# Performance work log

Measured on AMD Instinct MI355X. Metric: run time of the kernel, lower is better.

Reference implementation:

```python
import jax, jax.numpy as jnp
import numpy as np

N = 32768          # number of points
K = 64             # max_num_neighbors
D = 3              # spatial dim (3x3 local frames)
R = 1.0            # radius
TARGET_DEG = 48.0  # desired mean neighborhood size


def _radius_graph_numpy(pos, r, k):
    """Padded radius neighbor search (mimics torch_cluster.radius, incl. self-loop).

    Returns (edge_src, edge_dst, num_neighbors); padded slots have src == dst so
    edge_vec = 0 and they contribute nothing to the covariance scatter.
    """
    n = pos.shape[0]
    nbr = np.full((n, k), -1, dtype=np.int64)
    r2 = r * r
    chunk = 2048
    for s in range(0, n, chunk):
        q = pos[s:s + chunk]                                   # [C, D]
        d2 = ((q[:, None, :] - pos[None, :, :]) ** 2).sum(-1)  # [C, N]
        d2m = np.where(d2 <= r2, d2, np.inf)
        idx = np.argpartition(d2m, k - 1, axis=1)[:, :k]       # k nearest candidates
        dsel = np.take_along_axis(d2m, idx, axis=1)
        nbr[s:s + chunk] = np.where(np.isfinite(dsel), idx, -1)
    num_neighbors = (nbr >= 0).sum(axis=1).astype(np.int32)
    edge_dst = np.repeat(np.arange(n, dtype=np.int64), k)
    edge_src = nbr.reshape(-1)
    edge_src = np.where(edge_src >= 0, edge_src, edge_dst)     # pad: src == dst
    return edge_src.astype(np.int32), edge_dst.astype(np.int32), num_neighbors


def setup_inputs() -> dict:
    rng = np.random.default_rng(0)
    # box size so that density * (4/3) pi r^3 ~= TARGET_DEG
    L = (N * (4.0 / 3.0) * np.pi * R ** 3 / TARGET_DEG) ** (1.0 / 3.0)
    pos = rng.uniform(0.0, L, size=(N, D)).astype(np.float32)
    edge_src, edge_dst, num_neighbors = _radius_graph_numpy(pos, R, K)
    return {
        "pos": jnp.asarray(pos),
        "edge_src": jnp.asarray(edge_src),
        "edge_dst": jnp.asarray(edge_dst),
        "num_neighbors": jnp.asarray(num_neighbors),
    }


def reference(pos, edge_src, edge_dst, num_neighbors):
    n = pos.shape[0]
    # edge_vec = pos[col] - pos[row]; padded edges (src==dst) give exact zeros
    ev = pos[edge_src] - pos[edge_dst]                         # [E, 3]
    outer = ev[:, :, None] * ev[:, None, :]                    # [E, 3, 3]
    cov = jax.ops.segment_sum(outer, edge_dst, num_segments=n)  # [N, 3, 3]

    no_nbr = num_neighbors <= 1                                # self-loop only
    # replace degenerate (zero) covariances with a distinct-eigenvalue matrix so
    # eigh is well-defined; these rows are zeroed afterwards (exceptional 'zero').
    safe = jnp.diag(jnp.arange(1.0, D + 1.0, dtype=pos.dtype))
    cov = jnp.where(no_nbr[:, None, None], safe, cov)

    _, vecs = jnp.linalg.eigh(cov)                             # [N, 3, 3] columns = eigvecs
    frames = vecs.transpose(0, 2, 1)                           # rows = eigvecs
    frames = jnp.where(no_nbr[:, None, None], 0.0, frames)
    return frames


if __name__ == "__main__":
    out = reference(**setup_inputs())
    print(out.shape, out.dtype)
```

## Files before the change

kernel.cpp:

```cpp
#include <hip/hip_runtime.h>
#include <math.h>


#pragma clang fp contract(off)

#define EPS_F32    5.9604645e-8f
#define SAFMIN_F32 1.17549435e-38f

__device__ __forceinline__ float lapy2f(float x, float y) {
#pragma clang fp contract(off)
  float xa = fabsf(x), ya = fabsf(y);
  float w = fmaxf(xa, ya);
  float z = fminf(xa, ya);
  if (z == 0.0f) return w;
  float t = z / w;
  return w * sqrtf(1.0f + t * t);
}

__device__ __forceinline__ void slartgf(float f, float g, float* c, float* s, float* r) {
#pragma clang fp contract(off)
  const float safmin = SAFMIN_F32;
  const float safmax = 8.50705917e37f;
  const float rtmin  = 1.08420217e-19f;
  const float rtmax  = 6.52530446e18f;
  if (g == 0.0f) { *c = 1.0f; *s = 0.0f; *r = f; return; }
  if (f == 0.0f) { *c = 0.0f; *s = copysignf(1.0f, g); *r = fabsf(g); return; }
  float f1 = fabsf(f), g1 = fabsf(g);
  if (f1 > rtmin && f1 < rtmax && g1 > rtmin && g1 < rtmax) {
    float d = sqrtf(f * f + g * g);
    *c = f1 / d;
    *r = copysignf(d, f);
    *s = g / (*r);
  } else {
    float u  = fminf(safmax, fmaxf(safmin, fmaxf(f1, g1)));
    float fs = f / u, gs = g / u;
    float d  = sqrtf(fs * fs + gs * gs);
    *c = fabsf(fs) / d;
    float rr = copysignf(d, f);
    *s = gs / rr;
    *r = rr * u;
  }
}

__device__ __forceinline__ void slaev2f(float a, float b, float c,
                                        float* rt1, float* rt2,
                                        float* cs1, float* sn1) {
#pragma clang fp contract(off)
  float sm  = a + c;
  float df  = a - c;
  float adf = fabsf(df);
  float tb  = b + b;
  float ab  = fabsf(tb);
  float acmx, acmn;
  if (fabsf(a) > fabsf(c)) { acmx = a; acmn = c; } else { acmx = c; acmn = a; }
  float rt;
  if (adf > ab)      { float t = ab / adf; rt = adf * sqrtf(1.0f + t * t); }
  else if (adf < ab) { float t = adf / ab; rt = ab  * sqrtf(1.0f + t * t); }
  else               { rt = ab * sqrtf(2.0f); }
  int sgn1;
  if (sm < 0.0f) {
    *rt1 = 0.5f * (sm - rt); sgn1 = -1;
    *rt2 = (acmx / *rt1) * acmn - (b / *rt1) * b;
  } else if (sm > 0.0f) {
    *rt1 = 0.5f * (sm + rt); sgn1 = 1;
    *rt2 = (acmx / *rt1) * acmn - (b / *rt1) * b;
  } else {
    *rt1 = 0.5f * rt; *rt2 = -0.5f * rt; sgn1 = 1;
  }
  int sgn2; float cs;
  if (df >= 0.0f) { cs = df + rt; sgn2 = 1; }
  else            { cs = df - rt; sgn2 = -1; }
  float acs = fabsf(cs);
  if (acs > ab) {
    float ct = -tb / cs;
    *sn1 = 1.0f / sqrtf(1.0f + ct * ct);
    *cs1 = ct * (*sn1);
  } else {
    if (ab == 0.0f) { *cs1 = 1.0f; *sn1 = 0.0f; }
    else {
      float tn = -cs / tb;
      *cs1 = 1.0f / sqrtf(1.0f + tn * tn);
      *sn1 = tn * (*cs1);
    }
  }
  if (sgn1 == sgn2) { float tn = *cs1; *cs1 = -(*sn1); *sn1 = tn; }
}

template <int STR>
__device__ void ssteqr3(float* S) {
#pragma clang fp contract(off)
#define D_(i)   S[((i)-1)*STR]
#define E_(i)   S[(3+(i)-1)*STR]
#define Z_(i,j) S[(5+((i)-1)*3+((j)-1))*STR]
#define WC_(q)  S[(14+(q))*STR]
#define WS_(q)  S[(16+(q))*STR]
  const int   n      = 3;
  const float eps    = EPS_F32;
  const float eps2   = eps * eps;
  const float safmin = SAFMIN_F32;
  const float ssfmax = sqrtf(8.50705917e37f) / 3.0f;
  const float ssfmin = sqrtf(safmin) / eps2;

  int   l1, l, m, lsv, lend, lendsv, iscale, nmaxit, jtot;
  float anorm, p, g, r, rt1, rt2, c, s, f, b;

  for (int q = 0; q < 9; ++q) S[(5 + q) * STR] = 0.0f;
  Z_(1, 1) = 1.0f; Z_(2, 2) = 1.0f; Z_(3, 3) = 1.0f;

  nmaxit = n * 30;
  jtot   = 0;
  l1     = 1;

L10:
  if (l1 > n) goto L160;
  if (l1 > 1) E_(l1 - 1) = 0.0f;
  if (l1 <= n - 1) {
    for (m = l1; m <= n - 1; m++) {
      float tst = fabsf(E_(m));
      if (tst == 0.0f) goto L30;
      if (tst <= (sqrtf(fabsf(D_(m))) * sqrtf(fabsf(D_(m + 1)))) * eps) {
        E_(m) = 0.0f;
        goto L30;
      }
    }
  }
  m = n;
L30:
  l = l1; lsv = l; lend = m; lendsv = lend; l1 = m + 1;
  if (lend == l) goto L10;

  anorm = 0.0f;
  for (int q = l; q <= lend; q++)     anorm = fmaxf(anorm, fabsf(D_(q)));
  for (int q = l; q <= lend - 1; q++) anorm = fmaxf(anorm, fabsf(E_(q)));
  iscale = 0;
  if (anorm == 0.0f) goto L10;
  if (anorm > ssfmax) {
    iscale = 1;
    float sc = ssfmax / anorm;
    for (int q = l; q <= lend; q++)     D_(q) *= sc;
    for (int q = l; q <= lend - 1; q++) E_(q) *= sc;
  } else if (anorm < ssfmin) {
    iscale = 2;
    float sc = ssfmin / anorm;
    for (int q = l; q <= lend; q++)     D_(q) *= sc;
    for (int q = l; q <= lend - 1; q++) E_(q) *= sc;
  }

  if (fabsf(D_(lend)) < fabsf(D_(l))) { lend = lsv; l = lendsv; }

  if (lend > l) {
L40:
    if (l != lend) {
      for (m = l; m <= lend - 1; m++) {
        float tst = E_(m) * E_(m);
        if (tst <= (eps2 * fabsf(D_(m))) * fabsf(D_(m + 1)) + safmin) goto L60;
      }
    }
    m = lend;
L60:
    if (m < lend) E_(m) = 0.0f;
    p = D_(l);
    if (m == l) goto L80;
    if (m == l + 1) {
      slaev2f(D_(l), E_(l), D_(l + 1), &rt1, &rt2, &c, &s);
      WC_(l - 1) = c;
      WS_(l - 1) = s;
      for (int row = 1; row <= n; row++) {
        float t = Z_(row, l + 1);
        Z_(row, l + 1) = c * t - s * Z_(row, l);
        Z_(row, l)     = s * t + c * Z_(row, l);
      }
      D_(l) = rt1; D_(l + 1) = rt2; E_(l) = 0.0f;
      l += 2;
      if (l <= lend) goto L40;
      goto L140;
    }
    if (jtot == nmaxit) goto L140;
    jtot++;
    g = (D_(l + 1) - p) / (2.0f * E_(l));
    r = lapy2f(g, 1.0f);
    g = D_(m) - p + (E_(l) / (g + copysignf(r, g)));
    s = 1.0f; c = 1.0f; p = 0.0f;
    for (int i = m - 1; i >= l; i--) {
      f = s * E_(i);
      b = c * E_(i);
      slartgf(g, f, &c, &s, &r);
      if (i != m - 1) E_(i + 1) = r;
      g = D_(i + 1) - p;
      r = (D_(i) - g) * s + 2.0f * c * b;
      p = s * r;
      D_(i + 1) = g + p;
      g = c * r - b;
      WC_(i - 1) = c;
      WS_(i - 1) = -s;
    }
    {
      int mm = m - l + 1;
      for (int j = mm - 1; j >= 1; j--) {
        float cj = WC_(l + j - 2);
        float sj = WS_(l + j - 2);
        if (cj != 1.0f || sj != 0.0f) {
          int col = l + j - 1;
          for (int row = 1; row <= n; row++) {
            float t = Z_(row, col + 1);
            Z_(row, col + 1) = cj * t - sj * Z_(row, col);
            Z_(row, col)     = sj * t + cj * Z_(row, col);
          }
        }
      }
    }
    D_(l) = D_(l) - p;
    E_(l) = g;
    goto L40;
L80:
    D_(l) = p;
    l++;
    if (l <= lend) goto L40;
    goto L140;
  } else {
L90:
    if (l != lend) {
      for (m = l; m >= lend + 1; m--) {
        float tst = E_(m - 1) * E_(m - 1);
        if (tst <= (eps2 * fabsf(D_(m))) * fabsf(D_(m - 1)) + safmin) goto L110;
      }
    }
    m = lend;
L110:
    if (m > lend) E_(m - 1) = 0.0f;
    p = D_(l);
    if (m == l) goto L130;
    if (m == l - 1) {
      slaev2f(D_(l - 1), E_(l - 1), D_(l), &rt1, &rt2, &c, &s);
      WC_(m - 1) = c;
      WS_(m - 1) = s;
      for (int row = 1; row <= n; row++) {
        float t = Z_(row, l);
        Z_(row, l)     = c * t - s * Z_(row, l - 1);
        Z_(row, l - 1) = s * t + c * Z_(row, l - 1);
      }
      D_(l - 1) = rt1; D_(l) = rt2; E_(l - 1) = 0.0f;
      l -= 2;
      if (l >= lend) goto L90;
      goto L140;
    }
    if (jtot == nmaxit) goto L140;
    jtot++;
    g = (D_(l - 1) - p) / (2.0f * E_(l - 1));
    r = lapy2f(g, 1.0f);
    g = D_(m) - p + (E_(l - 1) / (g + copysignf(r, g)));
    s = 1.0f; c = 1.0f; p = 0.0f;
    for (int i = m; i <= l - 1; i++) {
      f = s * E_(i);
      b = c * E_(i);
      slartgf(g, f, &c, &s, &r);
      if (i != m) E_(i - 1) = r;
      g = D_(i) - p;
      r = (D_(i + 1) - g) * s + 2.0f * c * b;
      p = s * r;
      D_(i) = g + p;
      g = c * r - b;
      WC_(i - 1) = c;
      WS_(i - 1) = s;
    }
    {
      int mm = l - m + 1;
      for (int j = 1; j <= mm - 1; j++) {
        float cj = WC_(m + j - 2);
        float sj = WS_(m + j - 2);
        if (cj != 1.0f || sj != 0.0f) {
          int col = m + j - 1;
          for (int row = 1; row <= n; row++) {
            float t = Z_(row, col + 1);
            Z_(row, col + 1) = cj * t - sj * Z_(row, col);
            Z_(row, col)     = sj * t + cj * Z_(row, col);
          }
        }
      }
    }
    D_(l) = D_(l) - p;
    E_(l - 1) = g;
    goto L90;
L130:
    D_(l) = p;
    l--;
    if (l >= lend) goto L90;
    goto L140;
  }

L140:
  if (iscale == 1) {
    float sc = anorm / ssfmax;
    for (int q = lsv; q <= lendsv; q++)     D_(q) *= sc;
    for (int q = lsv; q <= lendsv - 1; q++) E_(q) *= sc;
  } else if (iscale == 2) {
    float sc = anorm / ssfmin;
    for (int q = lsv; q <= lendsv; q++)     D_(q) *= sc;
    for (int q = lsv; q <= lendsv - 1; q++) E_(q) *= sc;
  }
  if (jtot < nmaxit) goto L10;
  goto L160;

L160:
  for (int ii = 2; ii <= n; ii++) {
    int i = ii - 1, kk = i;
    p = D_(i);
    for (int j = ii; j <= n; j++) {
      if (D_(j) < p) { kk = j; p = D_(j); }
    }
    if (kk != i) {
      D_(kk) = D_(i);
      D_(i)  = p;
      for (int row = 1; row <= n; row++) {
        float t = Z_(row, i);
        Z_(row, i)  = Z_(row, kk);
        Z_(row, kk) = t;
      }
    }
  }
#undef D_
#undef E_
#undef Z_
#undef WC_
#undef WS_
}

template <int STR>
__device__ __forceinline__ void eig_frames(float c00, float c01, float c02,
                                           float c11, float c12, float c22,
                                           float* __restrict__ o, float* S) {
#pragma clang fp contract(off)
#define SZ(idx) S[(5 + (idx)) * STR]
  float tau1, v2;
  {
    float a11 = c00, a21 = c01, a31 = c02, a22 = c11, a32 = c12, a33 = c22;
    float xnorm = fabsf(a31);
    if (xnorm == 0.0f) {
      tau1 = 0.0f; v2 = 0.0f;
      S[0 * STR] = a11; S[1 * STR] = a22; S[2 * STR] = a33;
      S[3 * STR] = a21; S[4 * STR] = a32;
    } else {
      float py2  = lapy2f(a21, xnorm);
      float beta = -copysignf(py2, a21);
      tau1 = (beta - a21) / beta;
      v2   = a31 * (1.0f / (a21 - beta));
      float t2 = a32 * v2;
      float w1 = __builtin_fmaf(tau1, t2, tau1 * a22);
      float w2 = __builtin_fmaf(tau1 * v2, a33, tau1 * a32);
      float dot = __builtin_fmaf(v2, w2, w1);
      float ac = (-0.5f * tau1) * dot;
      w1 = w1 + ac;
      w2 = __builtin_fmaf(ac, v2, w2);
      float A11 = a22 - w1;
      A11 = A11 - w1;
      float A21 = a32 - w2;
      A21 = __builtin_fmaf(-w1, v2, A21);
      float A33 = __builtin_fmaf(-v2, w2, a33);
      A33 = __builtin_fmaf(-w2, v2, A33);
      S[0 * STR] = a11;
      S[1 * STR] = A11;
      S[4 * STR] = A21;
      S[2 * STR] = A33;
      S[3 * STR] = beta;
    }
  }

  ssteqr3<STR>(S);

  if (tau1 != 0.0f) {
    #pragma unroll
    for (int j = 0; j < 3; ++j) {
      float z2 = SZ(3 + j), z3 = SZ(6 + j);
      float w  = z2 + z3 * v2;
      float t  = tau1 * w;
      SZ(3 + j) = __builtin_fmaf(-tau1, w, z2);
      SZ(6 + j) = __builtin_fmaf(v2, -t, z3);
    }
  }

  o[0] = SZ(0); o[1] = SZ(3); o[2] = SZ(6);
  o[3] = SZ(1); o[4] = SZ(4); o[5] = SZ(7);
  o[6] = SZ(2); o[7] = SZ(5); o[8] = SZ(8);
#undef SZ
}

#define NODES_PER_BLOCK 64
#define NODE_STRIDE     193
#define SOLVER_LANES    16

__global__ void __launch_bounds__(256)
pca_frames_tiled_kernel(const float* __restrict__ pos,
                        const int*   __restrict__ esrc,
                        const int*   __restrict__ nn,
                        float*       __restrict__ out,
                        int n)
{
#pragma clang fp contract(off)
  __shared__ float sev[NODES_PER_BLOCK * NODE_STRIDE];
  __shared__ float sstate[4 * 18 * SOLVER_LANES];

  const int tid   = threadIdx.x;
  const int node0 = blockIdx.x * NODES_PER_BLOCK;

  const int ebase = blockIdx.x * (NODES_PER_BLOCK * 64);
  #pragma unroll
  for (int q = 0; q < 16; ++q) {
    int eb  = q * 256 + tid;
    int n_b = eb >> 6;
    int j   = eb & 63;
    int i   = node0 + n_b;
    int s   = esrc[ebase + eb];
    float dx = pos[3 * s + 0] - pos[3 * i + 0];
    float dy = pos[3 * s + 1] - pos[3 * i + 1];
    float dz = pos[3 * s + 2] - pos[3 * i + 2];
    float* row = sev + n_b * NODE_STRIDE + 3 * j;
    row[0] = dx;
    row[1] = dy;
    row[2] = dz;
  }

  __syncthreads();

  const int w = tid >> 6;
  const int l = tid & 63;
  if (l < SOLVER_LANES) {
    int nb = w * SOLVER_LANES + l;
    int i  = node0 + nb;
    float* o = out + (size_t)i * 9;

    if (nn[i] <= 1) {
      #pragma unroll
      for (int j = 0; j < 9; ++j) o[j] = 0.0f;
      return;
    }

    const float* row = sev + nb * NODE_STRIDE;
    float c00 = 0.0f, c01 = 0.0f, c02 = 0.0f, c11 = 0.0f, c12 = 0.0f, c22 = 0.0f;
    for (int j = 0; j < 64; ++j) {
      float dx = row[3 * j + 0];
      float dy = row[3 * j + 1];
      float dz = row[3 * j + 2];
      c00 = c00 + dx * dx;
      c01 = c01 + dx * dy;
      c02 = c02 + dx * dz;
      c11 = c11 + dy * dy;
      c12 = c12 + dy * dz;
      c22 = c22 + dz * dz;
    }

    float* S = sstate + w * (18 * SOLVER_LANES) + l;
    eig_frames<SOLVER_LANES>(c00, c01, c02, c11, c12, c22, o, S);
  }
}

__global__ void __launch_bounds__(64)
pca_frames_fused_kernel(const float* __restrict__ pos,
                        const int*   __restrict__ esrc,
                        const int*   __restrict__ nn,
                        float*       __restrict__ out,
                        int n, int k)
{
#pragma clang fp contract(off)
  __shared__ float fstate[64 * 18];
  int i = blockIdx.x * blockDim.x + threadIdx.x;
  if (i >= n) return;
  float* o = out + (size_t)i * 9;

  if (nn[i] <= 1) {
    #pragma unroll
    for (int j = 0; j < 9; ++j) o[j] = 0.0f;
    return;
  }

  float px = pos[3 * i + 0], py = pos[3 * i + 1], pz = pos[3 * i + 2];
  float c00 = 0.0f, c01 = 0.0f, c02 = 0.0f, c11 = 0.0f, c12 = 0.0f, c22 = 0.0f;
  const int* ep = esrc + (size_t)i * k;
  for (int j = 0; j < k; ++j) {
    int sidx = ep[j];
    float dx = pos[3 * sidx + 0] - px;
    float dy = pos[3 * sidx + 1] - py;
    float dz = pos[3 * sidx + 2] - pz;
    c00 = c00 + dx * dx;
    c01 = c01 + dx * dy;
    c02 = c02 + dx * dz;
    c11 = c11 + dy * dy;
    c12 = c12 + dy * dz;
    c22 = c22 + dz * dz;
  }

  float* S = fstate + threadIdx.x;
  eig_frames<64>(c00, c01, c02, c11, c12, c22, o, S);
}

extern "C" void kernel_launch(void* const* d_in, const int* in_sizes, int n_in,
                              void* d_out, int out_size, void* d_ws, size_t ws_size,
                              hipStream_t stream) {
  const float* pos  = (const float*)d_in[0];
  const int*   esrc = (const int*)d_in[1];
  const int*   nn   = (const int*)d_in[3];
  float*       out  = (float*)d_out;

  int n = in_sizes[0] / 3;
  if (n <= 0) return;
  int k = in_sizes[1] / n;

  if (k == 64 && (n % NODES_PER_BLOCK) == 0) {
    hipLaunchKernelGGL(pca_frames_tiled_kernel, dim3(n / NODES_PER_BLOCK),
                       dim3(256), 0, stream, pos, esrc, nn, out, n);
  } else {
    const int block = 64;
    hipLaunchKernelGGL(pca_frames_fused_kernel, dim3((n + block - 1) / block),
                       dim3(block), 0, stream, pos, esrc, nn, out, n, k);
  }
}
```

Baseline: 104.6 us.

## Keep 3x3 tridiagonal QL eigen-solver state in registers instead of shared memory

Rewrites the ssteqr-style 3x3 eigen-solver so D, E, Z and the rotation buffers live in scalar registers, selected through ternary macros, instead of strided shared-memory slots. This removes the per-thread shared-memory state arrays and the LDS traffic inside the iterative solver. It also loads the neighbor position as one 12-byte struct. The dynamic indices become select chains, which can add ALU work and raise register pressure.

Measured after the change: 115.4 us. 10.3% more time.

```diff
diff --git a/kernel.cpp b/kernel.cpp
--- a/kernel.cpp
+++ b/kernel.cpp
@@ -86,259 +86,18 @@
   if (sgn1 == sgn2) { float tn = *cs1; *cs1 = -(*sn1); *sn1 = tn; }
 }
 
-template <int STR>
-__device__ void ssteqr3(float* S) {
-#pragma clang fp contract(off)
-#define D_(i)   S[((i)-1)*STR]
-#define E_(i)   S[(3+(i)-1)*STR]
-#define Z_(i,j) S[(5+((i)-1)*3+((j)-1))*STR]
-#define WC_(q)  S[(14+(q))*STR]
-#define WS_(q)  S[(16+(q))*STR]
-  const int   n      = 3;
-  const float eps    = EPS_F32;
-  const float eps2   = eps * eps;
-  const float safmin = SAFMIN_F32;
-  const float ssfmax = sqrtf(8.50705917e37f) / 3.0f;
-  const float ssfmin = sqrtf(safmin) / eps2;
-
-  int   l1, l, m, lsv, lend, lendsv, iscale, nmaxit, jtot;
-  float anorm, p, g, r, rt1, rt2, c, s, f, b;
-
-  for (int q = 0; q < 9; ++q) S[(5 + q) * STR] = 0.0f;
-  Z_(1, 1) = 1.0f; Z_(2, 2) = 1.0f; Z_(3, 3) = 1.0f;
-
-  nmaxit = n * 30;
-  jtot   = 0;
-  l1     = 1;
-
-L10:
-  if (l1 > n) goto L160;
-  if (l1 > 1) E_(l1 - 1) = 0.0f;
-  if (l1 <= n - 1) {
-    for (m = l1; m <= n - 1; m++) {
-      float tst = fabsf(E_(m));
-      if (tst == 0.0f) goto L30;
-      if (tst <= (sqrtf(fabsf(D_(m))) * sqrtf(fabsf(D_(m + 1)))) * eps) {
-        E_(m) = 0.0f;
-        goto L30;
-      }
-    }
-  }
-  m = n;
-L30:
-  l = l1; lsv = l; lend = m; lendsv = lend; l1 = m + 1;
-  if (lend == l) goto L10;
-
-  anorm = 0.0f;
-  for (int q = l; q <= lend; q++)     anorm = fmaxf(anorm, fabsf(D_(q)));
-  for (int q = l; q <= lend - 1; q++) anorm = fmaxf(anorm, fabsf(E_(q)));
-  iscale = 0;
-  if (anorm == 0.0f) goto L10;
-  if (anorm > ssfmax) {
-    iscale = 1;
-    float sc = ssfmax / anorm;
-    for (int q = l; q <= lend; q++)     D_(q) *= sc;
-    for (int q = l; q <= lend - 1; q++) E_(q) *= sc;
-  } else if (anorm < ssfmin) {
-    iscale = 2;
-    float sc = ssfmin / anorm;
-    for (int q = l; q <= lend; q++)     D_(q) *= sc;
-    for (int q = l; q <= lend - 1; q++) E_(q) *= sc;
-  }
-
-  if (fabsf(D_(lend)) < fabsf(D_(l))) { lend = lsv; l = lendsv; }
-
-  if (lend > l) {
-L40:
-    if (l != lend) {
-      for (m = l; m <= lend - 1; m++) {
-        float tst = E_(m) * E_(m);
-        if (tst <= (eps2 * fabsf(D_(m))) * fabsf(D_(m + 1)) + safmin) goto L60;
-      }
-    }
-    m = lend;
-L60:
-    if (m < lend) E_(m) = 0.0f;
-    p = D_(l);
-    if (m == l) goto L80;
-    if (m == l + 1) {
-      slaev2f(D_(l), E_(l), D_(l + 1), &rt1, &rt2, &c, &s);
-      WC_(l - 1) = c;
-      WS_(l - 1) = s;
-      for (int row = 1; row <= n; row++) {
-        float t = Z_(row, l + 1);
-        Z_(row, l + 1) = c * t - s * Z_(row, l);
-        Z_(row, l)     = s * t + c * Z_(row, l);
-      }
-      D_(l) = rt1; D_(l + 1) = rt2; E_(l) = 0.0f;
-      l += 2;
-      if (l <= lend) goto L40;
-      goto L140;
-    }
-    if (jtot == nmaxit) goto L140;
-    jtot++;
-    g = (D_(l + 1) - p) / (2.0f * E_(l));
-    r = lapy2f(g, 1.0f);
-    g = D_(m) - p + (E_(l) / (g + copysignf(r, g)));
-    s = 1.0f; c = 1.0f; p = 0.0f;
-    for (int i = m - 1; i >= l; i--) {
-      f = s * E_(i);
-      b = c * E_(i);
-      slartgf(g, f, &c, &s, &r);
-      if (i != m - 1) E_(i + 1) = r;
-      g = D_(i + 1) - p;
-      r = (D_(i) - g) * s + 2.0f * c * b;
-      p = s * r;
-      D_(i + 1) = g + p;
-      g = c * r - b;
-      WC_(i - 1) = c;
-      WS_(i - 1) = -s;
-    }
-    {
-      int mm = m - l + 1;
-      for (int j = mm - 1; j >= 1; j--) {
-        float cj = WC_(l + j - 2);
-        float sj = WS_(l + j - 2);
-        if (cj != 1.0f || sj != 0.0f) {
-          int col = l + j - 1;
-          for (int row = 1; row <= n; row++) {
-            float t = Z_(row, col + 1);
-            Z_(row, col + 1) = cj * t - sj * Z_(row, col);
-            Z_(row, col)     = sj * t + cj * Z_(row, col);
-          }
-        }
-      }
-    }
-    D_(l) = D_(l) - p;
-    E_(l) = g;
-    goto L40;
-L80:
-    D_(l) = p;
-    l++;
-    if (l <= lend) goto L40;
-    goto L140;
-  } else {
-L90:
-    if (l != lend) {
-      for (m = l; m >= lend + 1; m--) {
-        float tst = E_(m - 1) * E_(m - 1);
-        if (tst <= (eps2 * fabsf(D_(m))) * fabsf(D_(m - 1)) + safmin) goto L110;
-      }
-    }
-    m = lend;
-L110:
-    if (m > lend) E_(m - 1) = 0.0f;
-    p = D_(l);
-    if (m == l) goto L130;
-    if (m == l - 1) {
-      slaev2f(D_(l - 1), E_(l - 1), D_(l), &rt1, &rt2, &c, &s);
-      WC_(m - 1) = c;
-      WS_(m - 1) = s;
-      for (int row = 1; row <= n; row++) {
-        float t = Z_(row, l);
-        Z_(row, l)     = c * t - s * Z_(row, l - 1);
-        Z_(row, l - 1) = s * t + c * Z_(row, l - 1);
-      }
-      D_(l - 1) = rt1; D_(l) = rt2; E_(l - 1) = 0.0f;
-      l -= 2;
-      if (l >= lend) goto L90;
-      goto L140;
-    }
-    if (jtot == nmaxit) goto L140;
-    jtot++;
-    g = (D_(l - 1) - p) / (2.0f * E_(l - 1));
-    r = lapy2f(g, 1.0f);
-    g = D_(m) - p + (E_(l - 1) / (g + copysignf(r, g)));
-    s = 1.0f; c = 1.0f; p = 0.0f;
-    for (int i = m; i <= l - 1; i++) {
-      f = s * E_(i);
-      b = c * E_(i);
-      slartgf(g, f, &c, &s, &r);
-      if (i != m) E_(i - 1) = r;
-      g = D_(i) - p;
-      r = (D_(i + 1) - g) * s + 2.0f * c * b;
-      p = s * r;
-      D_(i) = g + p;
-      g = c * r - b;
-      WC_(i - 1) = c;
-      WS_(i - 1) = s;
-    }
-    {
-      int mm = l - m + 1;
-      for (int j = 1; j <= mm - 1; j++) {
-        float cj = WC_(m + j - 2);
-        float sj = WS_(m + j - 2);
-        if (cj != 1.0f || sj != 0.0f) {
-          int col = m + j - 1;
-          for (int row = 1; row <= n; row++) {
-            float t = Z_(row, col + 1);
-            Z_(row, col + 1) = cj * t - sj * Z_(row, col);
-            Z_(row, col)     = sj * t + cj * Z_(row, col);
-          }
-        }
-      }
-    }
-    D_(l) = D_(l) - p;
-    E_(l - 1) = g;
-    goto L90;
-L130:
-    D_(l) = p;
-    l--;
-    if (l >= lend) goto L90;
-    goto L140;
-  }
-
-L140:
-  if (iscale == 1) {
-    float sc = anorm / ssfmax;
-    for (int q = lsv; q <= lendsv; q++)     D_(q) *= sc;
-    for (int q = lsv; q <= lendsv - 1; q++) E_(q) *= sc;
-  } else if (iscale == 2) {
-    float sc = anorm / ssfmin;
-    for (int q = lsv; q <= lendsv; q++)     D_(q) *= sc;
-    for (int q = lsv; q <= lendsv - 1; q++) E_(q) *= sc;
-  }
-  if (jtot < nmaxit) goto L10;
-  goto L160;
-
-L160:
-  for (int ii = 2; ii <= n; ii++) {
-    int i = ii - 1, kk = i;
-    p = D_(i);
-    for (int j = ii; j <= n; j++) {
-      if (D_(j) < p) { kk = j; p = D_(j); }
-    }
-    if (kk != i) {
-      D_(kk) = D_(i);
-      D_(i)  = p;
-      for (int row = 1; row <= n; row++) {
-        float t = Z_(row, i);
-        Z_(row, i)  = Z_(row, kk);
-        Z_(row, kk) = t;
-      }
-    }
-  }
-#undef D_
-#undef E_
-#undef Z_
-#undef WC_
-#undef WS_
-}
-
-template <int STR>
-__device__ __forceinline__ void eig_frames(float c00, float c01, float c02,
-                                           float c11, float c12, float c22,
-                                           float* __restrict__ o, float* S) {
-#pragma clang fp contract(off)
-#define SZ(idx) S[(5 + (idx)) * STR]
-  float tau1, v2;
+__device__ void eig_frames_reg(float c00, float c01, float c02,
+                               float c11, float c12, float c22,
+                               float* __restrict__ o) {
+#pragma clang fp contract(off)
+  float d1, d2, d3, e1, e2, tau1, v2;
   {
     float a11 = c00, a21 = c01, a31 = c02, a22 = c11, a32 = c12, a33 = c22;
     float xnorm = fabsf(a31);
     if (xnorm == 0.0f) {
       tau1 = 0.0f; v2 = 0.0f;
-      S[0 * STR] = a11; S[1 * STR] = a22; S[2 * STR] = a33;
-      S[3 * STR] = a21; S[4 * STR] = a32;
+      d1 = a11; d2 = a22; d3 = a33;
+      e1 = a21; e2 = a32;
     } else {
       float py2  = lapy2f(a21, xnorm);
       float beta = -copysignf(py2, a21);
@@ -357,36 +116,309 @@
       A21 = __builtin_fmaf(-w1, v2, A21);
       float A33 = __builtin_fmaf(-v2, w2, a33);
       A33 = __builtin_fmaf(-w2, v2, A33);
-      S[0 * STR] = a11;
-      S[1 * STR] = A11;
-      S[4 * STR] = A21;
-      S[2 * STR] = A33;
-      S[3 * STR] = beta;
-    }
-  }
-
-  ssteqr3<STR>(S);
+      d1 = a11; d2 = A11; d3 = A33;
+      e1 = beta; e2 = A21;
+    }
+  }
+
+  float z11 = 1.0f, z12 = 0.0f, z13 = 0.0f;
+  float z21 = 0.0f, z22 = 1.0f, z23 = 0.0f;
+  float z31 = 0.0f, z32 = 0.0f, z33 = 1.0f;
+  float wc0 = 0.0f, wc1 = 0.0f, ws0 = 0.0f, ws1 = 0.0f;
+
+#define DGET(i)    ((i) == 1 ? d1 : (i) == 2 ? d2 : d3)
+#define DSET(i,v)  do { float _t = (v); if ((i) == 1) d1 = _t; else if ((i) == 2) d2 = _t; else d3 = _t; } while (0)
+#define EGET(i)    ((i) == 1 ? e1 : e2)
+#define ESET(i,v)  do { float _t = (v); if ((i) == 1) e1 = _t; else e2 = _t; } while (0)
+#define WCGET(q)   ((q) == 0 ? wc0 : wc1)
+#define WCSET(q,v) do { float _t = (v); if ((q) == 0) wc0 = _t; else wc1 = _t; } while (0)
+#define WSGET(q)   ((q) == 0 ? ws0 : ws1)
+#define WSSET(q,v) do { float _t = (v); if ((q) == 0) ws0 = _t; else ws1 = _t; } while (0)
+#define ZGET(r,c)  ((r) == 1 ? ((c) == 1 ? z11 : (c) == 2 ? z12 : z13) \
+                  : (r) == 2 ? ((c) == 1 ? z21 : (c) == 2 ? z22 : z23) \
+                  :            ((c) == 1 ? z31 : (c) == 2 ? z32 : z33))
+#define ZSET(r,c,v) do { float _t = (v); \
+    if ((r) == 1)      { if ((c) == 1) z11 = _t; else if ((c) == 2) z12 = _t; else z13 = _t; } \
+    else if ((r) == 2) { if ((c) == 1) z21 = _t; else if ((c) == 2) z22 = _t; else z23 = _t; } \
+    else               { if ((c) == 1) z31 = _t; else if ((c) == 2) z32 = _t; else z33 = _t; } } while (0)
+
+  {
+    const float eps    = EPS_F32;
+    const float eps2   = eps * eps;
+    const float safmin = SAFMIN_F32;
+    const float ssfmax = sqrtf(8.50705917e37f) / 3.0f;
+    const float ssfmin = sqrtf(safmin) / eps2;
+
+    int   l1, l, m, lsv, lend, lendsv, iscale;
+    const int nmaxit = 90;
+    int   jtot = 0;
+    float anorm, p, g, r, rt1, rt2, rc, rs, f, b;
+
+    l1 = 1;
+
+L10:
+    if (l1 > 3) goto L160;
+    if (l1 > 1) ESET(l1 - 1, 0.0f);
+    if (l1 <= 2) {
+      for (m = l1; m <= 2; m++) {
+        float tst = fabsf(EGET(m));
+        if (tst == 0.0f) goto L30;
+        if (tst <= (sqrtf(fabsf(DGET(m))) * sqrtf(fabsf(DGET(m + 1)))) * eps) {
+          ESET(m, 0.0f);
+          goto L30;
+        }
+      }
+    }
+    m = 3;
+L30:
+    l = l1; lsv = l; lend = m; lendsv = lend; l1 = m + 1;
+    if (lend == l) goto L10;
+
+    anorm = 0.0f;
+    for (int q = l; q <= lend; q++)     anorm = fmaxf(anorm, fabsf(DGET(q)));
+    for (int q = l; q <= lend - 1; q++) anorm = fmaxf(anorm, fabsf(EGET(q)));
+    iscale = 0;
+    if (anorm == 0.0f) goto L10;
+    if (anorm > ssfmax) {
+      iscale = 1;
+      float sc = ssfmax / anorm;
+      for (int q = l; q <= lend; q++)     DSET(q, DGET(q) * sc);
+      for (int q = l; q <= lend - 1; q++) ESET(q, EGET(q) * sc);
+    } else if (anorm < ssfmin) {
+      iscale = 2;
+      float sc = ssfmin / anorm;
+      for (int q = l; q <= lend; q++)     DSET(q, DGET(q) * sc);
+      for (int q = l; q <= lend - 1; q++) ESET(q, EGET(q) * sc);
+    }
+
+    if (fabsf(DGET(lend)) < fabsf(DGET(l))) { lend = lsv; l = lendsv; }
+
+    if (lend > l) {
+L40:
+      if (l != lend) {
+        for (m = l; m <= lend - 1; m++) {
+          float tst = EGET(m) * EGET(m);
+          if (tst <= (eps2 * fabsf(DGET(m))) * fabsf(DGET(m + 1)) + safmin) goto L60;
+        }
+      }
+      m = lend;
+L60:
+      if (m < lend) ESET(m, 0.0f);
+      p = DGET(l);
+      if (m == l) goto L80;
+      if (m == l + 1) {
+        slaev2f(DGET(l), EGET(l), DGET(l + 1), &rt1, &rt2, &rc, &rs);
+        WCSET(l - 1, rc);
+        WSSET(l - 1, rs);
+        #pragma unroll
+        for (int row = 1; row <= 3; row++) {
+          float t  = ZGET(row, l + 1);
+          float zl = ZGET(row, l);
+          ZSET(row, l + 1, rc * t - rs * zl);
+          ZSET(row, l,     rs * t + rc * zl);
+        }
+        DSET(l, rt1); DSET(l + 1, rt2); ESET(l, 0.0f);
+        l += 2;
+        if (l <= lend) goto L40;
+        goto L140;
+      }
+      if (jtot == nmaxit) goto L140;
+      jtot++;
+      g = (DGET(l + 1) - p) / (2.0f * EGET(l));
+      r = lapy2f(g, 1.0f);
+      g = DGET(m) - p + (EGET(l) / (g + copysignf(r, g)));
+      rs = 1.0f; rc = 1.0f; p = 0.0f;
+      for (int i = m - 1; i >= l; i--) {
+        f = rs * EGET(i);
+        b = rc * EGET(i);
+        slartgf(g, f, &rc, &rs, &r);
+        if (i != m - 1) ESET(i + 1, r);
+        g = DGET(i + 1) - p;
+        r = (DGET(i) - g) * rs + 2.0f * rc * b;
+        p = rs * r;
+        DSET(i + 1, g + p);
+        g = rc * r - b;
+        WCSET(i - 1, rc);
+        WSSET(i - 1, -rs);
+      }
+      {
+        int mm = m - l + 1;
+        for (int j = mm - 1; j >= 1; j--) {
+          float cj = WCGET(l + j - 2);
+          float sj = WSGET(l + j - 2);
+          if (cj != 1.0f || sj != 0.0f) {
+            int col = l + j - 1;
+            #pragma unroll
+            for (int row = 1; row <= 3; row++) {
+              float t  = ZGET(row, col + 1);
+              float zc = ZGET(row, col);
+              ZSET(row, col + 1, cj * t - sj * zc);
+              ZSET(row, col,     sj * t + cj * zc);
+            }
+          }
+        }
+      }
+      DSET(l, DGET(l) - p);
+      ESET(l, g);
+      goto L40;
+L80:
+      DSET(l, p);
+      l++;
+      if (l <= lend) goto L40;
+      goto L140;
+    } else {
+L90:
+      if (l != lend) {
+        for (m = l; m >= lend + 1; m--) {
+          float tst = EGET(m - 1) * EGET(m - 1);
+          if (tst <= (eps2 * fabsf(DGET(m))) * fabsf(DGET(m - 1)) + safmin) goto L110;
+        }
+      }
+      m = lend;
+L110:
+      if (m > lend) ESET(m - 1, 0.0f);
+      p = DGET(l);
+      if (m == l) goto L130;
+      if (m == l - 1) {
+        slaev2f(DGET(l - 1), EGET(l - 1), DGET(l), &rt1, &rt2, &rc, &rs);
+        WCSET(m - 1, rc);
+        WSSET(m - 1, rs);
+        #pragma unroll
+        for (int row = 1; row <= 3; row++) {
+          float t  = ZGET(row, l);
+          float zl = ZGET(row, l - 1);
+          ZSET(row, l,     rc * t - rs * zl);
+          ZSET(row, l - 1, rs * t + rc * zl);
+        }
+        DSET(l - 1, rt1); DSET(l, rt2); ESET(l - 1, 0.0f);
+        l -= 2;
+        if (l >= lend) goto L90;
+        goto L140;
+      }
+      if (jtot == nmaxit) goto L140;
+      jtot++;
+      g = (DGET(l - 1) - p) / (2.0f * EGET(l - 1));
+      r = lapy2f(g, 1.0f);
+      g = DGET(m) - p + (EGET(l - 1) / (g + copysignf(r, g)));
+      rs = 1.0f; rc = 1.0f; p = 0.0f;
+      for (int i = m; i <= l - 1; i++) {
+        f = rs * EGET(i);
+        b = rc * EGET(i);
+        slartgf(g, f, &rc, &rs, &r);
+        if (i != m) ESET(i - 1, r);
+        g = DGET(i) - p;
+        r = (DGET(i + 1) - g) * rs + 2.0f * rc * b;
+        p = rs * r;
+        DSET(i, g + p);
+        g = rc * r - b;
+        WCSET(i - 1, rc);
+        WSSET(i - 1, rs);
+      }
+      {
+        int mm = l - m + 1;
+        for (int j = 1; j <= mm - 1; j++) {
+          float cj = WCGET(m + j - 2);
+          float sj = WSGET(m + j - 2);
+          if (cj != 1.0f || sj != 0.0f) {
+            int col = m + j - 1;
+            #pragma unroll
+            for (int row = 1; row <= 3; row++) {
+              float t  = ZGET(row, col + 1);
+              float zc = ZGET(row, col);
+              ZSET(row, col + 1, cj * t - sj * zc);
+              ZSET(row, col,     sj * t + cj * zc);
+            }
+          }
+        }
+      }
+      DSET(l, DGET(l) - p);
+      ESET(l - 1, g);
+      goto L90;
+L130:
+      DSET(l, p);
+      l--;
+      if (l >= lend) goto L90;
+      goto L140;
+    }
+
+L140:
+    if (iscale == 1) {
+      float sc = anorm / ssfmax;
+      for (int q = lsv; q <= lendsv; q++)     DSET(q, DGET(q) * sc);
+      for (int q = lsv; q <= lendsv - 1; q++) ESET(q, EGET(q) * sc);
+    } else if (iscale == 2) {
+      float sc = anorm / ssfmin;
+      for (int q = lsv; q <= lendsv; q++)     DSET(q, DGET(q) * sc);
+      for (int q = lsv; q <= lendsv - 1; q++) ESET(q, EGET(q) * sc);
+    }
+    if (jtot < nmaxit) goto L10;
+    goto L160;
+
+L160:
+    for (int ii = 2; ii <= 3; ii++) {
+      int i = ii - 1, kk = i;
+      p = DGET(i);
+      for (int j = ii; j <= 3; j++) {
+        if (DGET(j) < p) { kk = j; p = DGET(j); }
+      }
+      if (kk != i) {
+        DSET(kk, DGET(i));
+        DSET(i, p);
+        #pragma unroll
+        for (int row = 1; row <= 3; row++) {
+          float t = ZGET(row, i);
+          ZSET(row, i, ZGET(row, kk));
+          ZSET(row, kk, t);
+        }
+      }
+    }
+  }
+
+#undef DGET
+#undef DSET
+#undef EGET
+#undef ESET
+#undef WCGET
+#undef WCSET
+#undef WSGET
+#undef WSSET
+#undef ZGET
+#undef ZSET
 
   if (tau1 != 0.0f) {
-    #pragma unroll
-    for (int j = 0; j < 3; ++j) {
-      float z2 = SZ(3 + j), z3 = SZ(6 + j);
-      float w  = z2 + z3 * v2;
-      float t  = tau1 * w;
-      SZ(3 + j) = __builtin_fmaf(-tau1, w, z2);
-      SZ(6 + j) = __builtin_fmaf(v2, -t, z3);
-    }
-  }
-
-  o[0] = SZ(0); o[1] = SZ(3); o[2] = SZ(6);
-  o[3] = SZ(1); o[4] = SZ(4); o[5] = SZ(7);
-  o[6] = SZ(2); o[7] = SZ(5); o[8] = SZ(8);
-#undef SZ
+    {
+      float z2 = z21, z3 = z31;
+      float w = z2 + z3 * v2;
+      float t = tau1 * w;
+      z21 = __builtin_fmaf(-tau1, w, z2);
+      z31 = __builtin_fmaf(v2, -t, z3);
+    }
+    {
+      float z2 = z22, z3 = z32;
+      float w = z2 + z3 * v2;
+      float t = tau1 * w;
+      z22 = __builtin_fmaf(-tau1, w, z2);
+      z32 = __builtin_fmaf(v2, -t, z3);
+    }
+    {
+      float z2 = z23, z3 = z33;
+      float w = z2 + z3 * v2;
+      float t = tau1 * w;
+      z23 = __builtin_fmaf(-tau1, w, z2);
+      z33 = __builtin_fmaf(v2, -t, z3);
+    }
+  }
+
+  o[0] = z11; o[1] = z21; o[2] = z31;
+  o[3] = z12; o[4] = z22; o[5] = z32;
+  o[6] = z13; o[7] = z23; o[8] = z33;
 }
 
 #define NODES_PER_BLOCK 64
 #define NODE_STRIDE     193
 #define SOLVER_LANES    16
+
+struct __attribute__((aligned(4))) f3 { float x, y, z; };
 
 __global__ void __launch_bounds__(256)
 pca_frames_tiled_kernel(const float* __restrict__ pos,
@@ -397,7 +429,6 @@
 {
 #pragma clang fp contract(off)
   __shared__ float sev[NODES_PER_BLOCK * NODE_STRIDE];
-  __shared__ float sstate[4 * 18 * SOLVER_LANES];
 
   const int tid   = threadIdx.x;
   const int node0 = blockIdx.x * NODES_PER_BLOCK;
@@ -410,9 +441,10 @@
     int j   = eb & 63;
     int i   = node0 + n_b;
     int s   = esrc[ebase + eb];
-    float dx = pos[3 * s + 0] - pos[3 * i + 0];
-    float dy = pos[3 * s + 1] - pos[3 * i + 1];
-    float dz = pos[3 * s + 2] - pos[3 * i + 2];
+    f3 ps   = *reinterpret_cast<const f3*>(pos + 3 * s);
+    float dx = ps.x - pos[3 * i + 0];
+    float dy = ps.y - pos[3 * i + 1];
+    float dz = ps.z - pos[3 * i + 2];
     float* row = sev + n_b * NODE_STRIDE + 3 * j;
     row[0] = dx;
     row[1] = dy;
@@ -448,8 +480,7 @@
       c22 = c22 + dz * dz;
     }
 
-    float* S = sstate + w * (18 * SOLVER_LANES) + l;
-    eig_frames<SOLVER_LANES>(c00, c01, c02, c11, c12, c22, o, S);
+    eig_frames_reg(c00, c01, c02, c11, c12, c22, o);
   }
 }
 
@@ -461,7 +492,6 @@
                         int n, int k)
 {
 #pragma clang fp contract(off)
-  __shared__ float fstate[64 * 18];
   int i = blockIdx.x * blockDim.x + threadIdx.x;
   if (i >= n) return;
   float* o = out + (size_t)i * 9;
@@ -488,8 +518,7 @@
     c22 = c22 + dz * dz;
   }
 
-  float* S = fstate + threadIdx.x;
-  eig_frames<64>(c00, c01, c02, c11, c12, c22, o, S);
+  eig_frames_reg(c00, c01, c02, c11, c12, c22, o);
 }
 
 extern "C" void kernel_launch(void* const* d_in, const int* in_sizes, int n_in,
```
